# Performance work log

Measured on AMD Instinct MI355X. Metric: run time of the kernel, lower is better.

Reference implementation:

```python
import jax, jax.numpy as jnp
import numpy as np

B = 131072
HIDDEN = 20
N_HID_LAYERS = 8  # 1 input layer (3->20) + 7 hidden (20->20), then head 20->2
G_GRAV = 9.81


def _xavier(key, fan_in, fan_out, shape):
    lim = float(np.sqrt(6.0 / (fan_in + fan_out)))
    return jax.random.uniform(key, shape, jnp.float32, -lim, lim)


def setup_inputs() -> dict:
    key = jax.random.key(0)
    ks = jax.random.split(key, 9)
    return {
        "x": jax.random.normal(ks[0], (B,), jnp.float32),
        "y": jax.random.normal(ks[1], (B,), jnp.float32),
        "t": jax.random.normal(ks[2], (B,), jnp.float32),
        "u": jax.random.normal(ks[3], (B,), jnp.float32),
        "v": jax.random.normal(ks[4], (B,), jnp.float32),
        "W_in": _xavier(ks[5], 3, HIDDEN, (3, HIDDEN)),
        "b_in": jnp.zeros((HIDDEN,), jnp.float32),
        "W_h": _xavier(ks[6], HIDDEN, HIDDEN, (N_HID_LAYERS - 1, HIDDEN, HIDDEN)),
        "b_h": jnp.zeros((N_HID_LAYERS - 1, HIDDEN), jnp.float32),
        "W_out": _xavier(ks[7], HIDDEN, 2, (HIDDEN, 2)),
        "b_out": jnp.zeros((2,), jnp.float32),
        "lambda1": jnp.zeros((), jnp.float32),
        "lambda2": jnp.zeros((), jnp.float32),
    }


def _pinn(x, y, t, u, v, W_in, b_in, W_h, b_h, W_out, b_out, lambda1, lambda2):
    def net(z):  # z: (3,) -> (2,) = (psi, p)
        h = jnp.tanh(z @ W_in + b_in)
        for i in range(W_h.shape[0]):
            h = jnp.tanh(h @ W_h[i] + b_h[i])
        return h @ W_out + b_out

    psi_fn = lambda z: net(z)[0]
    p_fn = lambda z: net(z)[1]

    def per_point(z):
        G = jax.grad(psi_fn)(z)                       # (3,)  dpsi/dz
        H = jax.jacfwd(jax.grad(psi_fn))(z)           # (3,3) d2psi
        T = jax.jacfwd(jax.jacfwd(jax.grad(psi_fn)))(z)  # (3,3,3) d3psi
        return G, H, T, p_fn(z), jax.grad(p_fn)(z)

    z = jnp.stack([x, y, t], axis=1)  # (B,3), axes: 0=x, 1=y, 2=t
    G, H, T, p_pred, Gp = jax.vmap(per_point)(z)

    u_pred = G[:, 1]          # dpsi/dy
    v_pred = -G[:, 0]         # -dpsi/dx
    u_x, u_y, u_t = H[:, 1, 0], H[:, 1, 1], H[:, 1, 2]
    v_x, v_y, v_t = -H[:, 0, 0], -H[:, 0, 1], -H[:, 0, 2]
    u_xx, u_yy = T[:, 1, 0, 0], T[:, 1, 1, 1]
    v_xx, v_yy = -T[:, 0, 0, 0], -T[:, 0, 1, 1]
    p_x, p_y = Gp[:, 0], Gp[:, 1]

    f_u = lambda1 * (u_t + u_pred * u_x + v_pred * u_y) + p_x - lambda2 * (u_xx + u_yy)
    f_v = (lambda1 * (v_t + u_pred * v_x + v_pred * v_y) - lambda1 * G_GRAV
           + p_y - lambda2 * (v_xx + v_yy))

    preds = jnp.stack([p_pred, u_pred, v_pred], axis=1)  # (B,3)
    loss = (jnp.sum((u - u_pred) ** 2) + jnp.sum((v - v_pred) ** 2)
            + jnp.sum(f_u ** 2) + jnp.sum(f_v ** 2))
    return preds, loss


def reference(x, y, t, u, v, W_in, b_in, W_h, b_h, W_out, b_out, lambda1, lambda2):
    return _pinn(x, y, t, u, v, W_in, b_in, W_h, b_h, W_out, b_out, lambda1, lambda2)
```

## Files before the change

kernel.cpp:

```cpp
#include <hip/hip_runtime.h>

typedef float v2f __attribute__((ext_vector_type(2)));
typedef unsigned long long u64;
typedef unsigned int u32;

constexpr int BN   = 131072;
constexpr int HID  = 20;
constexpr int NLAY = 7;

constexpr int OFF_WH   = 0;
constexpr int OFF_BH   = 2800;
constexpr int OFF_WIN  = 2940;
constexpr int OFF_BIN  = 3000;
constexpr int OFF_WOUT = 3020;
constexpr int OFF_BOUT = 3060;
constexpr int LDS_TOT  = 3064;

enum { S_PX = 0, S_PXX, S_PXXX, S_P, S_GPX,
       S_PY, S_PYY, S_PYYY, S_GPY,
       S_D2P, S_D3P, S_D3M, S_XT, S_YT, NSLOT };

__device__ __forceinline__ float fast_tanh(float a) {
    float e = __builtin_amdgcn_exp2f(a * 2.8853900817779268f);
    float r = __builtin_amdgcn_rcpf(e + 1.0f);
    return __builtin_fmaf(-2.0f, r, 1.0f);
}
__device__ __forceinline__ v2f tanh2(v2f a) {
    v2f r; r.x = fast_tanh(a.x); r.y = fast_tanh(a.y); return r;
}
__device__ __forceinline__ v2f splat(float s) { v2f r = {s, s}; return r; }
#define FMA2(a, b, c) __builtin_elementwise_fma((a), (b), (c))

__device__ __forceinline__ float rdl(float v, int l) {
    return __int_as_float(__builtin_amdgcn_readlane(__float_as_int(v), l));
}
__device__ __forceinline__ u64 pack2(float lo, float hi) {
    return ((u64)(u32)__float_as_int(hi) << 32) | (u32)__float_as_int(lo);
}

__device__ __forceinline__ void pk_fma_lo(v2f& acc, const v2f s, const v2f w) {
    asm("v_pk_fma_f32 %0, %1, %2, %0 op_sel:[0,0,0] op_sel_hi:[0,1,1]"
        : "+v"(acc) : "v"(s), "v"(w));
}
__device__ __forceinline__ void pk_fma_hi(v2f& acc, const v2f s, const v2f w) {
    asm("v_pk_fma_f32 %0, %1, %2, %0 op_sel:[1,0,0] op_sel_hi:[1,1,1]"
        : "+v"(acc) : "v"(s), "v"(w));
}
__device__ __forceinline__ void pk_fma_hi_s(v2f& acc, const v2f s, const u64 w) {
    asm("v_pk_fma_f32 %0, %1, %2, %0 op_sel:[1,0,0] op_sel_hi:[1,1,1]"
        : "+v"(acc) : "v"(s), "s"(w));
}

__device__ __forceinline__ void stage_weights(
    float* smem, const float* Win, const float* bin, const float* Wh,
    const float* bh, const float* Wout, const float* bout)
{
    const int tid = threadIdx.x;
    for (int i = tid; i < 2800; i += 256) smem[OFF_WH + i] = Wh[i];
    for (int i = tid; i < 140;  i += 256) smem[OFF_BH + i] = bh[i];
    if (tid < 60) smem[OFF_WIN  + tid] = Win[tid];
    if (tid < 20) smem[OFF_BIN  + tid] = bin[tid];
    if (tid < 40) smem[OFF_WOUT + tid] = Wout[tid];
    if (tid < 2)  smem[OFF_BOUT + tid] = bout[tid];
    __syncthreads();
}

__global__ __launch_bounds__(256, 2) void pinn_fast6(
    const float* __restrict__ x, const float* __restrict__ y, const float* __restrict__ t,
    const float* __restrict__ u, const float* __restrict__ v,
    const float* __restrict__ Win, const float* __restrict__ bin,
    const float* __restrict__ Wh,  const float* __restrict__ bh,
    const float* __restrict__ Wout,const float* __restrict__ bout,
    const float* __restrict__ lam1p, const float* __restrict__ lam2p,
    float* __restrict__ out)
{
    if (lam1p[0] != 0.0f || lam2p[0] != 0.0f) return;

    __shared__ __align__(16) float smem[LDS_TOT];
    __shared__ __align__(8)  v2f  opair[NLAY * 128];
    __shared__ float wsum[4];

    const int tid  = threadIdx.x;
    const int lane = tid & 63;
    const int pt   = blockIdx.x * 256 + tid;

    const float xv = x[pt], yv = y[pt], tv = t[pt];
    const float uv = u[pt], vv = v[pt];

    for (int i = tid; i < 2800; i += 256) smem[OFF_WH + i] = Wh[i];
    if (tid < 60) smem[OFF_WIN  + tid] = Win[tid];
    if (tid < 20) smem[OFF_BIN  + tid] = bin[tid];
    if (tid < 40) smem[OFF_WOUT + tid] = Wout[tid];
    if (tid < 2)  smem[OFF_BOUT + tid] = bout[tid];
    for (int idx = tid; idx < NLAY * 128; idx += 256) {
        const int l = idx >> 7, q = idx & 127;
        if (q < 100) {
            const int i = q / 10, j = q % 10;
            opair[idx] = *(const v2f*)&Wh[l * 400 + (2 * i + 1) * 20 + 2 * j];
        } else if (q < 110) {
            const int j = q - 100;
            v2f b; b.x = bh[l * 20 + 2 * j]; b.y = bh[l * 20 + 2 * j + 1];
            opair[idx] = b;
        }
    }
    __syncthreads();

    v2f V[10], DX[10], DY[10];

    const v2f xv2 = splat(xv), yv2 = splat(yv), tv2 = splat(tv);
    #pragma unroll
    for (int j = 0; j < 10; ++j) {
        v2f w0 = *(const v2f*)&smem[OFF_WIN + 2*j];
        v2f w1 = *(const v2f*)&smem[OFF_WIN + HID + 2*j];
        v2f w2 = *(const v2f*)&smem[OFF_WIN + 2*HID + 2*j];
        v2f av = *(const v2f*)&smem[OFF_BIN + 2*j];
        av = FMA2(xv2, w0, av);
        av = FMA2(yv2, w1, av);
        av = FMA2(tv2, w2, av);
        v2f s  = tanh2(av);
        v2f s1 = 1.0f - s * s;
        V[j]  = s;
        DX[j] = s1 * w0;
        DY[j] = s1 * w1;
    }

    #pragma unroll 1
    for (int l = 0; l < NLAY; ++l) {
        const float* Wl = &smem[OFF_WH + l * 400];
        const v2f rc0 = opair[(l << 7) + lane];
        const v2f rc1 = opair[(l << 7) + 64 + lane];

        v2f aV[10], aX[10], aY[10];
        #pragma unroll
        for (int j = 0; j < 10; ++j) {
            v2f b; b.x = rdl(rc1.x, 36 + j); b.y = rdl(rc1.y, 36 + j);
            aV[j] = b;
            aX[j] = splat(0.f);
            aY[j] = splat(0.f);
        }

        #pragma unroll
        for (int i = 0; i < 10; ++i) {
            const float* r0 = &Wl[(2 * i) * HID];
            #pragma unroll
            for (int ob = 0; ob < 5; ++ob) {
                float4 w0 = *(const float4*)&r0[4 * ob];
                v2f w0a = {w0.x, w0.y}, w0b = {w0.z, w0.w};
                pk_fma_lo(aV[2*ob],   V[i],  w0a);
                pk_fma_lo(aV[2*ob+1], V[i],  w0b);
                pk_fma_lo(aX[2*ob],   DX[i], w0a);
                pk_fma_lo(aX[2*ob+1], DX[i], w0b);
                pk_fma_lo(aY[2*ob],   DY[i], w0a);
                pk_fma_lo(aY[2*ob+1], DY[i], w0b);
                const int q0 = i * 10 + 2 * ob, q1 = q0 + 1;
                const v2f cA = (q0 < 64) ? rc0 : rc1;
                const v2f cB = (q1 < 64) ? rc0 : rc1;
                const u64 wp0 = pack2(rdl(cA.x, q0 & 63), rdl(cA.y, q0 & 63));
                const u64 wp1 = pack2(rdl(cB.x, q1 & 63), rdl(cB.y, q1 & 63));
                pk_fma_hi_s(aV[2*ob],   V[i],  wp0);
                pk_fma_hi_s(aV[2*ob+1], V[i],  wp1);
                pk_fma_hi_s(aX[2*ob],   DX[i], wp0);
                pk_fma_hi_s(aX[2*ob+1], DX[i], wp1);
                pk_fma_hi_s(aY[2*ob],   DY[i], wp0);
                pk_fma_hi_s(aY[2*ob+1], DY[i], wp1);
            }
        }

        #pragma unroll
        for (int j = 0; j < 10; ++j) {
            v2f s  = tanh2(aV[j]);
            v2f s1 = 1.0f - s * s;
            V[j]  = s;
            DX[j] = s1 * aX[j];
            DY[j] = s1 * aY[j];
        }
    }

    v2f dX = splat(0.f), dY = splat(0.f), dP = splat(0.f),
        dPX = splat(0.f), dPY = splat(0.f);
    #pragma unroll
    for (int j = 0; j < 10; ++j) {
        v2f w0j = {smem[OFF_WOUT + 4*j],     smem[OFF_WOUT + 4*j + 2]};
        v2f w1j = {smem[OFF_WOUT + 4*j + 1], smem[OFF_WOUT + 4*j + 3]};
        dX  = FMA2(DX[j], w0j, dX);
        dY  = FMA2(DY[j], w0j, dY);
        dP  = FMA2(V[j],  w1j, dP);
        dPX = FMA2(DX[j], w1j, dPX);
        dPY = FMA2(DY[j], w1j, dPY);
    }
    const float psi_x = dX.x + dX.y;
    const float psi_y = dY.x + dY.y;
    const float pv    = smem[OFF_BOUT + 1] + dP.x + dP.y;
    const float p_x   = dPX.x + dPX.y;
    const float p_y   = dPY.x + dPY.y;

    out[3*pt+0] = pv;
    out[3*pt+1] = psi_y;
    out[3*pt+2] = -psi_x;

    const float du = uv - psi_y;
    const float dv = vv + psi_x;
    float term = du * du + dv * dv + p_x * p_x + p_y * p_y;

    #pragma unroll
    for (int off = 32; off > 0; off >>= 1) term += __shfl_down(term, off);
    const int wid = tid >> 6;
    if (lane == 0) wsum[wid] = term;
    __syncthreads();
    if (tid == 0) atomicAdd(&out[3*BN], wsum[0] + wsum[1] + wsum[2] + wsum[3]);
}

template<bool BIASED>
__device__ __forceinline__ void sweep2(const v2f (&S1)[10], const v2f (&S2)[10],
                                       v2f (&A1)[10], v2f (&A2)[10],
                                       const float* __restrict__ Wl,
                                       const float* __restrict__ bl)
{
    #pragma unroll
    for (int j = 0; j < 10; ++j) {
        if (BIASED) { A1[j].x = bl[2*j]; A1[j].y = bl[2*j+1]; }
        else        A1[j] = splat(0.f);
        A2[j] = splat(0.f);
    }
    #pragma unroll
    for (int i = 0; i < 10; ++i) {
        const float* r0 = &Wl[(2 * i) * HID];
        const float* r1 = &Wl[(2 * i + 1) * HID];
        #pragma unroll
        for (int ob = 0; ob < 5; ++ob) {
            float4 w0 = *(const float4*)&r0[4 * ob];
            float4 w1 = *(const float4*)&r1[4 * ob];
            v2f w0a = {w0.x, w0.y}, w0b = {w0.z, w0.w};
            v2f w1a = {w1.x, w1.y}, w1b = {w1.z, w1.w};
            pk_fma_lo(A1[2*ob],   S1[i], w0a);
            pk_fma_lo(A1[2*ob+1], S1[i], w0b);
            pk_fma_hi(A1[2*ob],   S1[i], w1a);
            pk_fma_hi(A1[2*ob+1], S1[i], w1b);
            pk_fma_lo(A2[2*ob],   S2[i], w0a);
            pk_fma_lo(A2[2*ob+1], S2[i], w0b);
            pk_fma_hi(A2[2*ob],   S2[i], w1a);
            pk_fma_hi(A2[2*ob+1], S2[i], w1b);
        }
    }
}

__global__ __launch_bounds__(256, 3) void pinn_jets6(
    const float* __restrict__ x, const float* __restrict__ y, const float* __restrict__ t,
    const float* __restrict__ Win, const float* __restrict__ bin,
    const float* __restrict__ Wh,  const float* __restrict__ bh,
    const float* __restrict__ Wout,const float* __restrict__ bout,
    const float* __restrict__ lam1p, const float* __restrict__ lam2p,
    float* __restrict__ ws)
{
    if (lam1p[0] == 0.0f && lam2p[0] == 0.0f) return;

    __shared__ __align__(16) float smem[LDS_TOT];
    stage_weights(smem, Win, bin, Wh, bh, Wout, bout);

    const int pt    = blockIdx.x * 256 + threadIdx.x;
    const int slice = blockIdx.y;

    const float xv = x[pt], yv = y[pt], tv = t[pt];
    const v2f xv2 = splat(xv), yv2 = splat(yv), tv2 = splat(tv);

    if (slice < 4) {
        const float DXT[4] = {1.f, 0.f, 1.f,  1.f};
        const float DYT[4] = {0.f, 1.f, 1.f, -1.f};
        const v2f dxv = splat(DXT[slice]), dyv = splat(DYT[slice]);

        v2f V[10], D1[10], D2[10], D3[10];

        #pragma unroll
        for (int j = 0; j < 10; ++j) {
            v2f w0 = *(const v2f*)&smem[OFF_WIN + 2*j];
            v2f w1 = *(const v2f*)&smem[OFF_WIN + HID + 2*j];
            v2f w2 = *(const v2f*)&smem[OFF_WIN + 2*HID + 2*j];
            v2f av = *(const v2f*)&smem[OFF_BIN + 2*j];
            av = FMA2(xv2, w0, av);
            av = FMA2(yv2, w1, av);
            av = FMA2(tv2, w2, av);
            v2f a1 = dxv * w0;
            a1 = FMA2(dyv, w1, a1);
            v2f s  = tanh2(av);
            v2f s2 = s * s;
            v2f s1 = 1.0f - s2;
            v2f f2 = -2.0f * s * s1;
            v2f f3 = s1 * (4.0f * s2 - 2.0f * s1);
            v2f a1sq = a1 * a1;
            V[j]  = s;
            D1[j] = s1 * a1;
            D2[j] = f2 * a1sq;
            D3[j] = f3 * a1sq * a1;
        }

        #pragma unroll 1
        for (int l = 0; l < NLAY; ++l) {
            const float* Wl = &smem[OFF_WH + l * (HID * HID)];
            const float* bl = &smem[OFF_BH + l * HID];
            v2f aV[10], a1[10];
            sweep2<true >(V,  D1, aV, a1, Wl, bl);
            v2f a2[10], a3[10];
            sweep2<false>(D2, D3, a2, a3, Wl, bl);
            #pragma unroll
            for (int j = 0; j < 10; ++j) {
                v2f s  = tanh2(aV[j]);
                v2f s2 = s * s;
                v2f s1 = 1.0f - s2;
                v2f f2 = -2.0f * s * s1;
                v2f f3 = s1 * (4.0f * s2 - 2.0f * s1);
                v2f u1 = a1[j];
                v2f u1sq = u1 * u1;
                V[j]  = s;
                D1[j] = s1 * u1;
                D2[j] = s1 * a2[j] + f2 * u1sq;
                D3[j] = s1 * a3[j] + 3.0f * f2 * (u1 * a2[j]) + f3 * u1sq * u1;
            }
        }

        v2f d1 = splat(0.f), d2 = splat(0.f), d3 = splat(0.f),
            dP = splat(0.f), dP1 = splat(0.f);
        #pragma unroll
        for (int j = 0; j < 10; ++j) {
            v2f w0j = {smem[OFF_WOUT + 4*j],     smem[OFF_WOUT + 4*j + 2]};
            v2f w1j = {smem[OFF_WOUT + 4*j + 1], smem[OFF_WOUT + 4*j + 3]};
            d1  = FMA2(D1[j], w0j, d1);
            d2  = FMA2(D2[j], w0j, d2);
            d3  = FMA2(D3[j], w0j, d3);
            dP  = FMA2(V[j],  w1j, dP);
            dP1 = FMA2(D1[j], w1j, dP1);
        }
        const float r1 = d1.x + d1.y;
        const float r2 = d2.x + d2.y;
        const float r3 = d3.x + d3.y;

        switch (slice) {
            case 0:
                ws[S_PX  *BN+pt] = r1;
                ws[S_PXX *BN+pt] = r2;
                ws[S_PXXX*BN+pt] = r3;
                ws[S_P   *BN+pt] = smem[OFF_BOUT + 1] + dP.x + dP.y;
                ws[S_GPX *BN+pt] = dP1.x + dP1.y;
                break;
            case 1:
                ws[S_PY  *BN+pt] = r1;
                ws[S_PYY *BN+pt] = r2;
                ws[S_PYYY*BN+pt] = r3;
                ws[S_GPY *BN+pt] = dP1.x + dP1.y;
                break;
            case 2:
                ws[S_D2P *BN+pt] = r2;
                ws[S_D3P *BN+pt] = r3;
                break;
            default:
                ws[S_D3M *BN+pt] = r3;
                break;
        }
    } else {
        v2f V[10], DA[10], DT[10], DAT[10];

        #pragma unroll
        for (int j = 0; j < 10; ++j) {
            v2f w0 = *(const v2f*)&smem[OFF_WIN + 2*j];
            v2f w1 = *(const v2f*)&smem[OFF_WIN + HID + 2*j];
            v2f w2 = *(const v2f*)&smem[OFF_WIN + 2*HID + 2*j];
            v2f av = *(const v2f*)&smem[OFF_BIN + 2*j];
            av = FMA2(xv2, w0, av);
            av = FMA2(yv2, w1, av);
            av = FMA2(tv2, w2, av);
            v2f wa = (slice == 4) ? w0 : w1;
            v2f s  = tanh2(av);
            v2f s1 = 1.0f - s * s;
            v2f f2 = -2.0f * s * s1;
            V[j]   = s;
            DA[j]  = s1 * wa;
            DT[j]  = s1 * w2;
            DAT[j] = f2 * wa * w2;
        }

        #pragma unroll 1
        for (int l = 0; l < NLAY; ++l) {
            const float* Wl = &smem[OFF_WH + l * (HID * HID)];
            const float* bl = &smem[OFF_BH + l * HID];
            v2f aV[10], aA[10];
            sweep2<true >(V,  DA,  aV, aA, Wl, bl);
            v2f aT[10], aAT[10];
            sweep2<false>(DT, DAT, aT, aAT, Wl, bl);
            #pragma unroll
            for (int j = 0; j < 10; ++j) {
                v2f s  = tanh2(aV[j]);
                v2f s1 = 1.0f - s * s;
                v2f f2 = -2.0f * s * s1;
                V[j]   = s;
                DA[j]  = s1 * aA[j];
                DT[j]  = s1 * aT[j];
                DAT[j] = f2 * (aA[j] * aT[j]) + s1 * aAT[j];
            }
        }

        v2f dAT = splat(0.f);
        #pragma unroll
        for (int j = 0; j < 10; ++j) {
            v2f w0j = {smem[OFF_WOUT + 4*j], smem[OFF_WOUT + 4*j + 2]};
            dAT = FMA2(DAT[j], w0j, dAT);
        }
        const float r = dAT.x + dAT.y;
        if (slice == 4) ws[S_XT*BN+pt] = r;
        else            ws[S_YT*BN+pt] = r;
    }
}

__global__ __launch_bounds__(256) void pinn_combine(
    const float* __restrict__ ws,
    const float* __restrict__ u, const float* __restrict__ v,
    const float* __restrict__ lam1p, const float* __restrict__ lam2p,
    float* __restrict__ out)
{
    if (lam1p[0] == 0.0f && lam2p[0] == 0.0f) return;

    __shared__ float wsum[4];
    const int tid = threadIdx.x;
    const int pt  = blockIdx.x * 256 + tid;

    const float psi_x   = ws[S_PX  *BN+pt];
    const float psi_xx  = ws[S_PXX *BN+pt];
    const float psi_xxx = ws[S_PXXX*BN+pt];
    const float pv      = ws[S_P   *BN+pt];
    const float p_x     = ws[S_GPX *BN+pt];
    const float psi_y   = ws[S_PY  *BN+pt];
    const float psi_yy  = ws[S_PYY *BN+pt];
    const float psi_yyy = ws[S_PYYY*BN+pt];
    const float p_y     = ws[S_GPY *BN+pt];
    const float d2p     = ws[S_D2P *BN+pt];
    const float d3p     = ws[S_D3P *BN+pt];
    const float d3m     = ws[S_D3M *BN+pt];
    const float psi_xt  = ws[S_XT  *BN+pt];
    const float psi_yt  = ws[S_YT  *BN+pt];

    const float psi_xy  = 0.5f * (d2p - psi_xx - psi_yy);
    const float psi_xxy = (d3p - d3m - 2.0f * psi_yyy) * (1.0f / 6.0f);
    const float psi_xyy = (d3p + d3m - 2.0f * psi_xxx) * (1.0f / 6.0f);

    const float u_pred = psi_y;
    const float v_pred = -psi_x;
    const float u_x = psi_xy,  u_y = psi_yy,  u_t = psi_yt;
    const float v_x = -psi_xx, v_y = -psi_xy, v_t = -psi_xt;
    const float u_xx = psi_xxy, u_yy = psi_yyy;
    const float v_xx = -psi_xxx, v_yy = -psi_xyy;

    const float lam1 = lam1p[0];
    const float lam2 = lam2p[0];

    const float f_u = lam1 * (u_t + u_pred * u_x + v_pred * u_y) + p_x - lam2 * (u_xx + u_yy);
    const float f_v = lam1 * (v_t + u_pred * v_x + v_pred * v_y) - lam1 * 9.81f + p_y
                      - lam2 * (v_xx + v_yy);

    out[3*pt+0] = pv;
    out[3*pt+1] = u_pred;
    out[3*pt+2] = v_pred;

    const float du = u[pt] - u_pred;
    const float dv = v[pt] - v_pred;
    float term = du * du + dv * dv + f_u * f_u + f_v * f_v;

    #pragma unroll
    for (int off = 32; off > 0; off >>= 1) term += __shfl_down(term, off);
    const int lane = tid & 63, wid = tid >> 6;
    if (lane == 0) wsum[wid] = term;
    __syncthreads();
    if (tid == 0) atomicAdd(&out[3*BN], wsum[0] + wsum[1] + wsum[2] + wsum[3]);
}

extern "C" void kernel_launch(void* const* d_in, const int* in_sizes, int n_in,
                              void* d_out, int out_size, void* d_ws, size_t ws_size,
                              hipStream_t stream) {
    const float* x    = (const float*)d_in[0];
    const float* y    = (const float*)d_in[1];
    const float* t    = (const float*)d_in[2];
    const float* u    = (const float*)d_in[3];
    const float* v    = (const float*)d_in[4];
    const float* Win  = (const float*)d_in[5];
    const float* bin  = (const float*)d_in[6];
    const float* Wh   = (const float*)d_in[7];
    const float* bh   = (const float*)d_in[8];
    const float* Wout = (const float*)d_in[9];
    const float* bout = (const float*)d_in[10];
    const float* lam1 = (const float*)d_in[11];
    const float* lam2 = (const float*)d_in[12];

    float* out = (float*)d_out;
    float* ws  = (float*)d_ws;

    hipMemsetAsync(out + 3 * BN, 0, sizeof(float), stream);

    pinn_fast6<<<BN / 256, 256, 0, stream>>>(x, y, t, u, v, Win, bin, Wh, bh,
                                             Wout, bout, lam1, lam2, out);
    pinn_jets6<<<dim3(BN / 256, 6), 256, 0, stream>>>(x, y, t, Win, bin, Wh, bh,
                                                      Wout, bout, lam1, lam2, ws);
    pinn_combine<<<BN / 256, 256, 0, stream>>>(ws, u, v, lam1, lam2, out);
}
```

Measured before the change: 48.03 us.

## Merge fast and jet kernels into one launch with prefetched LDS weights

Folds the lambda-zero fast path and the jet kernels into a single kernel, using blockIdx.y to choose the branch. This removes one kernel launch and the separate empty-exit dispatch. In the fast path, the readlane/SGPR packing of odd-row weights is dropped in favour of float4 LDS loads of both rows, software-prefetched one row pair ahead. Occupancy is pinned to two waves per EU. The trade-off is more LDS traffic and register pressure, plus six early-exiting block rows per column in the fast case.

```diff
diff --git a/kernel.cpp b/kernel.cpp
--- a/kernel.cpp
+++ b/kernel.cpp
@@ -1,8 +1,6 @@
 #include <hip/hip_runtime.h>
 
 typedef float v2f __attribute__((ext_vector_type(2)));
-typedef unsigned long long u64;
-typedef unsigned int u32;
 
 constexpr int BN   = 131072;
 constexpr int HID  = 20;
@@ -31,13 +29,6 @@
 __device__ __forceinline__ v2f splat(float s) { v2f r = {s, s}; return r; }
 #define FMA2(a, b, c) __builtin_elementwise_fma((a), (b), (c))
 
-__device__ __forceinline__ float rdl(float v, int l) {
-    return __int_as_float(__builtin_amdgcn_readlane(__float_as_int(v), l));
-}
-__device__ __forceinline__ u64 pack2(float lo, float hi) {
-    return ((u64)(u32)__float_as_int(hi) << 32) | (u32)__float_as_int(lo);
-}
-
 __device__ __forceinline__ void pk_fma_lo(v2f& acc, const v2f s, const v2f w) {
     asm("v_pk_fma_f32 %0, %1, %2, %0 op_sel:[0,0,0] op_sel_hi:[0,1,1]"
         : "+v"(acc) : "v"(s), "v"(w));
@@ -45,10 +36,6 @@
 __device__ __forceinline__ void pk_fma_hi(v2f& acc, const v2f s, const v2f w) {
     asm("v_pk_fma_f32 %0, %1, %2, %0 op_sel:[1,0,0] op_sel_hi:[1,1,1]"
         : "+v"(acc) : "v"(s), "v"(w));
-}
-__device__ __forceinline__ void pk_fma_hi_s(v2f& acc, const v2f s, const u64 w) {
-    asm("v_pk_fma_f32 %0, %1, %2, %0 op_sel:[1,0,0] op_sel_hi:[1,1,1]"
-        : "+v"(acc) : "v"(s), "s"(w));
 }
 
 __device__ __forceinline__ void stage_weights(
@@ -63,151 +50,6 @@
     if (tid < 40) smem[OFF_WOUT + tid] = Wout[tid];
     if (tid < 2)  smem[OFF_BOUT + tid] = bout[tid];
     __syncthreads();
-}
-
-__global__ __launch_bounds__(256, 2) void pinn_fast6(
-    const float* __restrict__ x, const float* __restrict__ y, const float* __restrict__ t,
-    const float* __restrict__ u, const float* __restrict__ v,
-    const float* __restrict__ Win, const float* __restrict__ bin,
-    const float* __restrict__ Wh,  const float* __restrict__ bh,
-    const float* __restrict__ Wout,const float* __restrict__ bout,
-    const float* __restrict__ lam1p, const float* __restrict__ lam2p,
-    float* __restrict__ out)
-{
-    if (lam1p[0] != 0.0f || lam2p[0] != 0.0f) return;
-
-    __shared__ __align__(16) float smem[LDS_TOT];
-    __shared__ __align__(8)  v2f  opair[NLAY * 128];
-    __shared__ float wsum[4];
-
-    const int tid  = threadIdx.x;
-    const int lane = tid & 63;
-    const int pt   = blockIdx.x * 256 + tid;
-
-    const float xv = x[pt], yv = y[pt], tv = t[pt];
-    const float uv = u[pt], vv = v[pt];
-
-    for (int i = tid; i < 2800; i += 256) smem[OFF_WH + i] = Wh[i];
-    if (tid < 60) smem[OFF_WIN  + tid] = Win[tid];
-    if (tid < 20) smem[OFF_BIN  + tid] = bin[tid];
-    if (tid < 40) smem[OFF_WOUT + tid] = Wout[tid];
-    if (tid < 2)  smem[OFF_BOUT + tid] = bout[tid];
-    for (int idx = tid; idx < NLAY * 128; idx += 256) {
-        const int l = idx >> 7, q = idx & 127;
-        if (q < 100) {
-            const int i = q / 10, j = q % 10;
-            opair[idx] = *(const v2f*)&Wh[l * 400 + (2 * i + 1) * 20 + 2 * j];
-        } else if (q < 110) {
-            const int j = q - 100;
-            v2f b; b.x = bh[l * 20 + 2 * j]; b.y = bh[l * 20 + 2 * j + 1];
-            opair[idx] = b;
-        }
-    }
-    __syncthreads();
-
-    v2f V[10], DX[10], DY[10];
-
-    const v2f xv2 = splat(xv), yv2 = splat(yv), tv2 = splat(tv);
-    #pragma unroll
-    for (int j = 0; j < 10; ++j) {
-        v2f w0 = *(const v2f*)&smem[OFF_WIN + 2*j];
-        v2f w1 = *(const v2f*)&smem[OFF_WIN + HID + 2*j];
-        v2f w2 = *(const v2f*)&smem[OFF_WIN + 2*HID + 2*j];
-        v2f av = *(const v2f*)&smem[OFF_BIN + 2*j];
-        av = FMA2(xv2, w0, av);
-        av = FMA2(yv2, w1, av);
-        av = FMA2(tv2, w2, av);
-        v2f s  = tanh2(av);
-        v2f s1 = 1.0f - s * s;
-        V[j]  = s;
-        DX[j] = s1 * w0;
-        DY[j] = s1 * w1;
-    }
-
-    #pragma unroll 1
-    for (int l = 0; l < NLAY; ++l) {
-        const float* Wl = &smem[OFF_WH + l * 400];
-        const v2f rc0 = opair[(l << 7) + lane];
-        const v2f rc1 = opair[(l << 7) + 64 + lane];
-
-        v2f aV[10], aX[10], aY[10];
-        #pragma unroll
-        for (int j = 0; j < 10; ++j) {
-            v2f b; b.x = rdl(rc1.x, 36 + j); b.y = rdl(rc1.y, 36 + j);
-            aV[j] = b;
-            aX[j] = splat(0.f);
-            aY[j] = splat(0.f);
-        }
-
-        #pragma unroll
-        for (int i = 0; i < 10; ++i) {
-            const float* r0 = &Wl[(2 * i) * HID];
-            #pragma unroll
-            for (int ob = 0; ob < 5; ++ob) {
-                float4 w0 = *(const float4*)&r0[4 * ob];
-                v2f w0a = {w0.x, w0.y}, w0b = {w0.z, w0.w};
-                pk_fma_lo(aV[2*ob],   V[i],  w0a);
-                pk_fma_lo(aV[2*ob+1], V[i],  w0b);
-                pk_fma_lo(aX[2*ob],   DX[i], w0a);
-                pk_fma_lo(aX[2*ob+1], DX[i], w0b);
-                pk_fma_lo(aY[2*ob],   DY[i], w0a);
-                pk_fma_lo(aY[2*ob+1], DY[i], w0b);
-                const int q0 = i * 10 + 2 * ob, q1 = q0 + 1;
-                const v2f cA = (q0 < 64) ? rc0 : rc1;
-                const v2f cB = (q1 < 64) ? rc0 : rc1;
-                const u64 wp0 = pack2(rdl(cA.x, q0 & 63), rdl(cA.y, q0 & 63));
-                const u64 wp1 = pack2(rdl(cB.x, q1 & 63), rdl(cB.y, q1 & 63));
-                pk_fma_hi_s(aV[2*ob],   V[i],  wp0);
-                pk_fma_hi_s(aV[2*ob+1], V[i],  wp1);
-                pk_fma_hi_s(aX[2*ob],   DX[i], wp0);
-                pk_fma_hi_s(aX[2*ob+1], DX[i], wp1);
-                pk_fma_hi_s(aY[2*ob],   DY[i], wp0);
-                pk_fma_hi_s(aY[2*ob+1], DY[i], wp1);
-            }
-        }
-
-        #pragma unroll
-        for (int j = 0; j < 10; ++j) {
-            v2f s  = tanh2(aV[j]);
-            v2f s1 = 1.0f - s * s;
-            V[j]  = s;
-            DX[j] = s1 * aX[j];
-            DY[j] = s1 * aY[j];
-        }
-    }
-
-    v2f dX = splat(0.f), dY = splat(0.f), dP = splat(0.f),
-        dPX = splat(0.f), dPY = splat(0.f);
-    #pragma unroll
-    for (int j = 0; j < 10; ++j) {
-        v2f w0j = {smem[OFF_WOUT + 4*j],     smem[OFF_WOUT + 4*j + 2]};
-        v2f w1j = {smem[OFF_WOUT + 4*j + 1], smem[OFF_WOUT + 4*j + 3]};
-        dX  = FMA2(DX[j], w0j, dX);
-        dY  = FMA2(DY[j], w0j, dY);
-        dP  = FMA2(V[j],  w1j, dP);
-        dPX = FMA2(DX[j], w1j, dPX);
-        dPY = FMA2(DY[j], w1j, dPY);
-    }
-    const float psi_x = dX.x + dX.y;
-    const float psi_y = dY.x + dY.y;
-    const float pv    = smem[OFF_BOUT + 1] + dP.x + dP.y;
-    const float p_x   = dPX.x + dPX.y;
-    const float p_y   = dPY.x + dPY.y;
-
-    out[3*pt+0] = pv;
-    out[3*pt+1] = psi_y;
-    out[3*pt+2] = -psi_x;
-
-    const float du = uv - psi_y;
-    const float dv = vv + psi_x;
-    float term = du * du + dv * dv + p_x * p_x + p_y * p_y;
-
-    #pragma unroll
-    for (int off = 32; off > 0; off >>= 1) term += __shfl_down(term, off);
-    const int wid = tid >> 6;
-    if (lane == 0) wsum[wid] = term;
-    __syncthreads();
-    if (tid == 0) atomicAdd(&out[3*BN], wsum[0] + wsum[1] + wsum[2] + wsum[3]);
 }
 
 template<bool BIASED>
@@ -244,24 +86,153 @@
     }
 }
 
-__global__ __launch_bounds__(256, 3) void pinn_jets6(
+__global__ __launch_bounds__(256)
+__attribute__((amdgpu_waves_per_eu(2, 2)))
+void pinn_main(
     const float* __restrict__ x, const float* __restrict__ y, const float* __restrict__ t,
+    const float* __restrict__ u, const float* __restrict__ v,
     const float* __restrict__ Win, const float* __restrict__ bin,
     const float* __restrict__ Wh,  const float* __restrict__ bh,
     const float* __restrict__ Wout,const float* __restrict__ bout,
     const float* __restrict__ lam1p, const float* __restrict__ lam2p,
-    float* __restrict__ ws)
+    float* __restrict__ ws, float* __restrict__ out)
 {
-    if (lam1p[0] == 0.0f && lam2p[0] == 0.0f) return;
+    const bool lam0 = (lam1p[0] == 0.0f && lam2p[0] == 0.0f);
+    if (blockIdx.y == 0) { if (!lam0) return; }
+    else                 { if (lam0)  return; }
 
     __shared__ __align__(16) float smem[LDS_TOT];
+    __shared__ float wsum[4];
+
+    const int tid = threadIdx.x;
+    const int pt  = blockIdx.x * 256 + tid;
+
+    const float xv = x[pt], yv = y[pt], tv = t[pt];
+    float uv = 0.f, vv = 0.f;
+    if (blockIdx.y == 0) { uv = u[pt]; vv = v[pt]; }
+
     stage_weights(smem, Win, bin, Wh, bh, Wout, bout);
 
-    const int pt    = blockIdx.x * 256 + threadIdx.x;
-    const int slice = blockIdx.y;
-
-    const float xv = x[pt], yv = y[pt], tv = t[pt];
     const v2f xv2 = splat(xv), yv2 = splat(yv), tv2 = splat(tv);
+
+    if (blockIdx.y == 0) {
+        v2f V[10], DX[10], DY[10];
+
+        #pragma unroll
+        for (int j = 0; j < 10; ++j) {
+            v2f w0 = *(const v2f*)&smem[OFF_WIN + 2*j];
+            v2f w1 = *(const v2f*)&smem[OFF_WIN + HID + 2*j];
+            v2f w2 = *(const v2f*)&smem[OFF_WIN + 2*HID + 2*j];
+            v2f av = *(const v2f*)&smem[OFF_BIN + 2*j];
+            av = FMA2(xv2, w0, av);
+            av = FMA2(yv2, w1, av);
+            av = FMA2(tv2, w2, av);
+            v2f s  = tanh2(av);
+            v2f s1 = 1.0f - s * s;
+            V[j]  = s;
+            DX[j] = s1 * w0;
+            DY[j] = s1 * w1;
+        }
+
+        #pragma unroll 1
+        for (int l = 0; l < NLAY; ++l) {
+            const float* Wl = &smem[OFF_WH + l * 400];
+            const float* bl = &smem[OFF_BH + l * HID];
+
+            v2f aV[10], aX[10], aY[10];
+            #pragma unroll
+            for (int j = 0; j < 10; ++j) {
+                aV[j].x = bl[2*j]; aV[j].y = bl[2*j+1];
+                aX[j] = splat(0.f);
+                aY[j] = splat(0.f);
+            }
+
+            float4 WE[5], WO[5];
+            #pragma unroll
+            for (int q = 0; q < 5; ++q) {
+                WE[q] = *(const float4*)&Wl[4 * q];
+                WO[q] = *(const float4*)&Wl[HID + 4 * q];
+            }
+
+            #pragma unroll
+            for (int i = 0; i < 10; ++i) {
+                float4 NE[5], NO[5];
+                if (i < 9) {
+                    #pragma unroll
+                    for (int q = 0; q < 5; ++q) {
+                        NE[q] = *(const float4*)&Wl[(2 * i + 2) * HID + 4 * q];
+                        NO[q] = *(const float4*)&Wl[(2 * i + 3) * HID + 4 * q];
+                    }
+                }
+                #pragma unroll
+                for (int ob = 0; ob < 5; ++ob) {
+                    v2f w0a = {WE[ob].x, WE[ob].y}, w0b = {WE[ob].z, WE[ob].w};
+                    v2f w1a = {WO[ob].x, WO[ob].y}, w1b = {WO[ob].z, WO[ob].w};
+                    pk_fma_lo(aV[2*ob],   V[i],  w0a);
+                    pk_fma_lo(aV[2*ob+1], V[i],  w0b);
+                    pk_fma_hi(aV[2*ob],   V[i],  w1a);
+                    pk_fma_hi(aV[2*ob+1], V[i],  w1b);
+                    pk_fma_lo(aX[2*ob],   DX[i], w0a);
+                    pk_fma_lo(aX[2*ob+1], DX[i], w0b);
+                    pk_fma_hi(aX[2*ob],   DX[i], w1a);
+                    pk_fma_hi(aX[2*ob+1], DX[i], w1b);
+                    pk_fma_lo(aY[2*ob],   DY[i], w0a);
+                    pk_fma_lo(aY[2*ob+1], DY[i], w0b);
+                    pk_fma_hi(aY[2*ob],   DY[i], w1a);
+                    pk_fma_hi(aY[2*ob+1], DY[i], w1b);
+                }
+                if (i < 9) {
+                    #pragma unroll
+                    for (int q = 0; q < 5; ++q) { WE[q] = NE[q]; WO[q] = NO[q]; }
+                }
+            }
+
+            #pragma unroll
+            for (int j = 0; j < 10; ++j) {
+                v2f s  = tanh2(aV[j]);
+                v2f s1 = 1.0f - s * s;
+                V[j]  = s;
+                DX[j] = s1 * aX[j];
+                DY[j] = s1 * aY[j];
+            }
+        }
+
+        v2f dX = splat(0.f), dY = splat(0.f), dP = splat(0.f),
+            dPX = splat(0.f), dPY = splat(0.f);
+        #pragma unroll
+        for (int j = 0; j < 10; ++j) {
+            v2f w0j = {smem[OFF_WOUT + 4*j],     smem[OFF_WOUT + 4*j + 2]};
+            v2f w1j = {smem[OFF_WOUT + 4*j + 1], smem[OFF_WOUT + 4*j + 3]};
+            dX  = FMA2(DX[j], w0j, dX);
+            dY  = FMA2(DY[j], w0j, dY);
+            dP  = FMA2(V[j],  w1j, dP);
+            dPX = FMA2(DX[j], w1j, dPX);
+            dPY = FMA2(DY[j], w1j, dPY);
+        }
+        const float psi_x = dX.x + dX.y;
+        const float psi_y = dY.x + dY.y;
+        const float pv    = smem[OFF_BOUT + 1] + dP.x + dP.y;
+        const float p_x   = dPX.x + dPX.y;
+        const float p_y   = dPY.x + dPY.y;
+
+        out[3*pt+0] = pv;
+        out[3*pt+1] = psi_y;
+        out[3*pt+2] = -psi_x;
+
+        const float du = uv - psi_y;
+        const float dv = vv + psi_x;
+        float term = du * du + dv * dv + p_x * p_x + p_y * p_y;
+
+        #pragma unroll
+        for (int off = 32; off > 0; off >>= 1) term += __shfl_down(term, off);
+        const int lane = tid & 63, wid = tid >> 6;
+        if (lane == 0) wsum[wid] = term;
+        __syncthreads();
+        if (tid == 0) atomicAdd(&out[3*BN], wsum[0] + wsum[1] + wsum[2] + wsum[3]);
+        return;
+    }
+
+    const int slice = blockIdx.y - 1;
 
     if (slice < 4) {
         const float DXT[4] = {1.f, 0.f, 1.f,  1.f};
@@ -492,9 +463,7 @@
 
     hipMemsetAsync(out + 3 * BN, 0, sizeof(float), stream);
 
-    pinn_fast6<<<BN / 256, 256, 0, stream>>>(x, y, t, u, v, Win, bin, Wh, bh,
-                                             Wout, bout, lam1, lam2, out);
-    pinn_jets6<<<dim3(BN / 256, 6), 256, 0, stream>>>(x, y, t, Win, bin, Wh, bh,
-                                                      Wout, bout, lam1, lam2, ws);
+    pinn_main<<<dim3(BN / 256, 7), 256, 0, stream>>>(x, y, t, u, v, Win, bin, Wh, bh,
+                                                     Wout, bout, lam1, lam2, ws, out);
     pinn_combine<<<BN / 256, 256, 0, stream>>>(ws, u, v, lam1, lam2, out);
 }
```

Result: faster. 43.10 us (-10.3%).
